# Kernel tuning notes

Hardware: AMD Instinct MI355X
Metric: run time of the kernel (lower is better)

The kernel has to match this reference:

```python
import jax, jax.numpy as jnp
import numpy as np

N_NODES = 100000
N_EDGES = 1250000
FEAT = 64
HID = 10
MOD = 10.0


def setup_inputs() -> dict:
    key = jax.random.key(0)
    ks = jax.random.split(key, 12)
    inp = {
        "X": jax.random.normal(ks[0], (N_NODES, FEAT), dtype=jnp.float32),
        "W2_0": jax.random.normal(ks[1], (2 * FEAT, HID), dtype=jnp.float32) * 0.1,
        "W1_0": jax.random.normal(ks[2], (HID, HID), dtype=jnp.float32) * 0.3,
        "W2_1": jax.random.normal(ks[3], (2 * HID, HID), dtype=jnp.float32) * 0.3,
        "W1_1": jax.random.normal(ks[4], (HID, HID), dtype=jnp.float32) * 0.3,
        "W2_2": jax.random.normal(ks[5], (2 * HID, HID), dtype=jnp.float32) * 0.3,
        "W1_2": jax.random.normal(ks[6], (HID, HID), dtype=jnp.float32) * 0.3,
        "Wf1": jax.random.normal(ks[7], (HID, FEAT), dtype=jnp.float32) * 0.3,
        "Wf2": jax.random.normal(ks[8], (FEAT, FEAT), dtype=jnp.float32) * 0.1,
        "edge_src": jax.random.randint(ks[9], (N_EDGES,), 0, N_NODES, dtype=jnp.int64 if jax.config.jax_enable_x64 else jnp.int32),
        "edge_dst": jax.random.randint(ks[10], (N_EDGES,), 0, N_NODES, dtype=jnp.int64 if jax.config.jax_enable_x64 else jnp.int32),
    }
    return inp


def _rgcn_layer(X, W2, W1, src, dst):
    # gather target (i) and source (j) node features per edge: [E, in_dim]
    X_i = X[dst]
    X_j = X[src]
    # message: dense_2(relu) then dense_1(relu), divided by mod
    m = jax.nn.relu(jnp.concatenate([X_i, X_j], axis=-1) @ W2)
    m = jax.nn.relu(m @ W1) / MOD  # [E, HID]
    # sum-aggregate messages at target nodes
    agg = jax.ops.segment_sum(m, dst, num_segments=N_NODES)
    # layer activation='relu' (identity here since messages are nonneg, kept for fidelity)
    return jax.nn.relu(agg)


def reference(X, W2_0, W1_0, W2_1, W1_1, W2_2, W1_2, Wf1, Wf2, edge_src, edge_dst):
    h = X
    for W2, W1 in ((W2_0, W1_0), (W2_1, W1_1), (W2_2, W1_2)):
        h = _rgcn_layer(h, W2, W1, edge_src, edge_dst)
    h = jax.nn.relu(h @ Wf1)
    h = jax.nn.relu(h @ Wf2)
    return h
```

## Files before the change

### kernel.cpp

```cpp
#include <hip/hip_runtime.h>

#define FEAT 64
#define HID 10
#define RS 16
#define EPB 1024
#define BSH 6
#define CHK 32

__global__ __launch_bounds__(256) void pre_l0(
    const float* __restrict__ X,
    const float* __restrict__ W2,
    float* __restrict__ A,
    float* __restrict__ B,
    int n_nodes)
{
    __shared__ float w2[128 * 10];
    for (int i = threadIdx.x; i < 1280; i += 256) w2[i] = W2[i];
    __syncthreads();

    int n = blockIdx.x * 256 + threadIdx.x;
    if (n >= n_nodes) return;

    const float4* xr = reinterpret_cast<const float4*>(X + (size_t)n * FEAT);
    float a[10], b[10];
#pragma unroll
    for (int h = 0; h < 10; h++) { a[h] = 0.f; b[h] = 0.f; }

#pragma unroll
    for (int blk = 0; blk < 16; blk++) {
        float4 u = xr[blk];
        float xv[4] = { u.x, u.y, u.z, u.w };
#pragma unroll
        for (int j = 0; j < 4; j++) {
            int k = blk * 4 + j;
#pragma unroll
            for (int h = 0; h < 10; h++) {
                a[h] = fmaf(xv[j], w2[k * 10 + h], a[h]);
                b[h] = fmaf(xv[j], w2[(64 + k) * 10 + h], b[h]);
            }
        }
    }

    float4* Ar = reinterpret_cast<float4*>(A + (size_t)n * RS);
    float4* Br = reinterpret_cast<float4*>(B + (size_t)n * RS);
    Ar[0] = make_float4(a[0], a[1], a[2], a[3]);
    Ar[1] = make_float4(a[4], a[5], a[6], a[7]);
    Ar[2] = make_float4(a[8], a[9], 0.f, 0.f);
    Br[0] = make_float4(b[0], b[1], b[2], b[3]);
    Br[1] = make_float4(b[4], b[5], b[6], b[7]);
    Br[2] = make_float4(b[8], b[9], 0.f, 0.f);
}

__global__ __launch_bounds__(256) void pre_small(
    const float* __restrict__ H,
    const float* __restrict__ W2,
    float* __restrict__ A,
    float* __restrict__ B,
    int n_nodes)
{
    __shared__ float w2[200];
    for (int i = threadIdx.x; i < 200; i += 256) w2[i] = W2[i];
    __syncthreads();

    int n = blockIdx.x * 256 + threadIdx.x;
    if (n >= n_nodes) return;

    const float4* hr = reinterpret_cast<const float4*>(H + (size_t)n * RS);
    float4 h0 = hr[0], h1 = hr[1], h2 = hr[2];
    float hv[10] = { h0.x, h0.y, h0.z, h0.w, h1.x, h1.y, h1.z, h1.w, h2.x, h2.y };

    float a[10], b[10];
#pragma unroll
    for (int h = 0; h < 10; h++) { a[h] = 0.f; b[h] = 0.f; }
#pragma unroll
    for (int k = 0; k < 10; k++) {
#pragma unroll
        for (int h = 0; h < 10; h++) {
            a[h] = fmaf(hv[k], w2[k * 10 + h], a[h]);
            b[h] = fmaf(hv[k], w2[(10 + k) * 10 + h], b[h]);
        }
    }

    float4* Ar = reinterpret_cast<float4*>(A + (size_t)n * RS);
    float4* Br = reinterpret_cast<float4*>(B + (size_t)n * RS);
    Ar[0] = make_float4(a[0], a[1], a[2], a[3]);
    Ar[1] = make_float4(a[4], a[5], a[6], a[7]);
    Ar[2] = make_float4(a[8], a[9], 0.f, 0.f);
    Br[0] = make_float4(b[0], b[1], b[2], b[3]);
    Br[1] = make_float4(b[4], b[5], b[6], b[7]);
    Br[2] = make_float4(b[8], b[9], 0.f, 0.f);
}


__global__ __launch_bounds__(256) void bin_hist_k(
    const int* __restrict__ dst, int* __restrict__ blockhist, int n_edges, int nbk)
{
    extern __shared__ int hist[];
    for (int i = threadIdx.x; i < nbk; i += 256) hist[i] = 0;
    __syncthreads();
    int base = blockIdx.x * EPB;
    for (int i = threadIdx.x; i < EPB; i += 256) {
        int e = base + i;
        if (e < n_edges) atomicAdd(&hist[dst[e] >> BSH], 1);
    }
    __syncthreads();
    int* row = blockhist + (size_t)blockIdx.x * nbk;
    for (int i = threadIdx.x; i < nbk; i += 256) row[i] = hist[i];
}

__global__ __launch_bounds__(256) void colchunk_sum_k(
    const int* __restrict__ blockhist, int* __restrict__ chunksum,
    int nbk, int nblk)
{
    int b = blockIdx.x * 256 + threadIdx.x;
    int c = blockIdx.y;
    if (b >= nbk) return;
    int k0 = c * CHK;
    int k1 = min(k0 + CHK, nblk);
    int s = 0;
    for (int k = k0; k < k1; k++) s += blockhist[(size_t)k * nbk + b];
    chunksum[(size_t)c * nbk + b] = s;
}

__global__ __launch_bounds__(256) void chunk_scan_k(
    int* __restrict__ chunksum, int* __restrict__ btot, int nbk, int nchk)
{
    int b = blockIdx.x * 256 + threadIdx.x;
    if (b >= nbk) return;
    int run = 0;
    for (int c = 0; c < nchk; c++) {
        size_t idx = (size_t)c * nbk + b;
        int v = chunksum[idx];
        chunksum[idx] = run;
        run += v;
    }
    btot[b] = run;
}

__global__ __launch_bounds__(256) void scan_k(
    const int* __restrict__ btot, int* __restrict__ bbase,
    int* __restrict__ bucket_start, int* __restrict__ start,
    int nbk, int n_nodes, int n_edges)
{
    __shared__ int ts[256];
    int t = threadIdx.x;
    int v[8];
    int s = 0;
#pragma unroll
    for (int j = 0; j < 8; j++) {
        int idx = t * 8 + j;
        v[j] = (idx < nbk) ? btot[idx] : 0;
        s += v[j];
    }
    ts[t] = s;
    __syncthreads();
    for (int off = 1; off < 256; off <<= 1) {
        int x = (t >= off) ? ts[t - off] : 0;
        __syncthreads();
        ts[t] += x;
        __syncthreads();
    }
    int run = ts[t] - s;
#pragma unroll
    for (int j = 0; j < 8; j++) {
        int idx = t * 8 + j;
        if (idx < nbk) { bbase[idx] = run; bucket_start[idx] = run; }
        run += v[j];
    }
    if (t == 255) { bucket_start[nbk] = n_edges; start[n_nodes] = n_edges; }
}

__global__ __launch_bounds__(256) void col_off2_k(
    int* __restrict__ blockhist, const int* __restrict__ chunksum,
    const int* __restrict__ bbase, int nbk, int nblk)
{
    int b = blockIdx.x * 256 + threadIdx.x;
    int c = blockIdx.y;
    if (b >= nbk) return;
    int k0 = c * CHK;
    int k1 = min(k0 + CHK, nblk);
    int run = bbase[b] + chunksum[(size_t)c * nbk + b];
    for (int k = k0; k < k1; k++) {
        size_t idx = (size_t)k * nbk + b;
        int v = blockhist[idx];
        blockhist[idx] = run;
        run += v;
    }
}

__global__ __launch_bounds__(256) void bin_scatter_k(
    const int* __restrict__ src, const int* __restrict__ dst,
    const int* __restrict__ blockhist, int* __restrict__ packed,
    int n_edges, int nbk)
{
    extern __shared__ int cur[];
    const int* row = blockhist + (size_t)blockIdx.x * nbk;
    for (int i = threadIdx.x; i < nbk; i += 256) cur[i] = row[i];
    __syncthreads();
    int base = blockIdx.x * EPB;
    for (int i = threadIdx.x; i < EPB; i += 256) {
        int e = base + i;
        if (e < n_edges) {
            int d = dst[e];
            int pos = atomicAdd(&cur[d >> BSH], 1);
            packed[pos] = ((d & 63) << 17) | src[e];
        }
    }
}

__global__ __launch_bounds__(256) void csr_k(
    const int* __restrict__ packed, const int* __restrict__ bucket_start,
    int* __restrict__ nbr, int* __restrict__ start, int n_nodes)
{
    __shared__ int hist[64];
    __shared__ int excl[64];
    __shared__ int cur[64];
    int b = blockIdx.x;
    int base = bucket_start[b];
    int end  = bucket_start[b + 1];
    if (threadIdx.x < 64) hist[threadIdx.x] = 0;
    __syncthreads();
    for (int i = base + threadIdx.x; i < end; i += 256)
        atomicAdd(&hist[packed[i] >> 17], 1);
    __syncthreads();
    if (threadIdx.x == 0) {
        int r = 0;
        for (int k = 0; k < 64; k++) { excl[k] = r; r += hist[k]; }
    }
    __syncthreads();
    if (threadIdx.x < 64) {
        cur[threadIdx.x] = excl[threadIdx.x];
        int node = (b << 6) + threadIdx.x;
        if (node < n_nodes) start[node] = base + excl[threadIdx.x];
    }
    __syncthreads();
    for (int i = base + threadIdx.x; i < end; i += 256) {
        int p = packed[i];
        int pos = base + atomicAdd(&cur[p >> 17], 1);
        nbr[pos] = p & 0x1FFFF;
    }
}

__global__ __launch_bounds__(256) void gather_k(
    const float* __restrict__ A,
    const float* __restrict__ B,
    const float* __restrict__ W1,
    const int* __restrict__ start,
    const int* __restrict__ nbr,
    float* __restrict__ H,
    int n_nodes)
{
    __shared__ float w1[100];
    for (int i = threadIdx.x; i < 100; i += 256) w1[i] = W1[i];
    __syncthreads();

    int t = blockIdx.x * 256 + threadIdx.x;
    int n = t >> 2;
    int q = t & 3;
    if (n >= n_nodes) return;

    const float4* ar = reinterpret_cast<const float4*>(A + (size_t)n * RS);
    float4 a0 = ar[0], a1 = ar[1], a2 = ar[2];
    float av[10] = { a0.x, a0.y, a0.z, a0.w, a1.x, a1.y, a1.z, a1.w, a2.x, a2.y };

    float acc[10];
#pragma unroll
    for (int h = 0; h < 10; h++) acc[h] = 0.f;

    int beg = start[n];
    int end = start[n + 1];
    for (int i = beg + q; i < end; i += 4) {
        int s = nbr[i];
        const float4* br = reinterpret_cast<const float4*>(B + (size_t)s * RS);
        float4 b0 = br[0], b1 = br[1], b2 = br[2];
        float pre[10] = { av[0] + b0.x, av[1] + b0.y, av[2] + b0.z, av[3] + b0.w,
                          av[4] + b1.x, av[5] + b1.y, av[6] + b1.z, av[7] + b1.w,
                          av[8] + b2.x, av[9] + b2.y };
#pragma unroll
        for (int j = 0; j < 10; j++) pre[j] = fmaxf(pre[j], 0.f);
#pragma unroll
        for (int h = 0; h < 10; h++) {
            float z = 0.f;
#pragma unroll
            for (int j = 0; j < 10; j++) z = fmaf(pre[j], w1[j * 10 + h], z);
            acc[h] += fmaxf(z, 0.f);
        }
    }

#pragma unroll
    for (int h = 0; h < 10; h++) acc[h] += __shfl_xor(acc[h], 1);
#pragma unroll
    for (int h = 0; h < 10; h++) acc[h] += __shfl_xor(acc[h], 2);

    if (q == 0) {
        float4* Hr = reinterpret_cast<float4*>(H + (size_t)n * RS);
        Hr[0] = make_float4(acc[0] * 0.1f, acc[1] * 0.1f, acc[2] * 0.1f, acc[3] * 0.1f);
        Hr[1] = make_float4(acc[4] * 0.1f, acc[5] * 0.1f, acc[6] * 0.1f, acc[7] * 0.1f);
        Hr[2] = make_float4(acc[8] * 0.1f, acc[9] * 0.1f, 0.f, 0.f);
    }
}

__global__ __launch_bounds__(256) void final_k(
    const float* __restrict__ H,
    const float* __restrict__ Wf1,
    const float* __restrict__ Wf2,
    float* __restrict__ out,
    int n_nodes)
{
    __shared__ float wf1[640];
    __shared__ float wf2s[64 * 64];
    __shared__ float tT[64 * 64];

    for (int i = threadIdx.x; i < 640; i += 256) wf1[i] = Wf1[i];
    {
        const float4* w2v = reinterpret_cast<const float4*>(Wf2);
        float4* w2s = reinterpret_cast<float4*>(wf2s);
        for (int i = threadIdx.x; i < 1024; i += 256) w2s[i] = w2v[i];
    }

    int node0 = blockIdx.x * 64;

    {
        int r = threadIdx.x & 63;
        int g = threadIdx.x >> 6;
        int node = node0 + r;
        float hv[10];
        if (node < n_nodes) {
            const float4* hr = reinterpret_cast<const float4*>(H + (size_t)node * RS);
            float4 h0 = hr[0], h1 = hr[1], h2 = hr[2];
            hv[0]=h0.x; hv[1]=h0.y; hv[2]=h0.z; hv[3]=h0.w;
            hv[4]=h1.x; hv[5]=h1.y; hv[6]=h1.z; hv[7]=h1.w;
            hv[8]=h2.x; hv[9]=h2.y;
        } else {
#pragma unroll
            for (int k = 0; k < 10; k++) hv[k] = 0.f;
        }
        __syncthreads();
#pragma unroll
        for (int j = 0; j < 16; j++) {
            int c = g * 16 + j;
            float v = 0.f;
#pragma unroll
            for (int k = 0; k < 10; k++) v = fmaf(hv[k], wf1[k * 64 + c], v);
            tT[c * 64 + r] = fmaxf(v, 0.f);
        }
    }
    __syncthreads();

    int r0 = (threadIdx.x >> 4) * 4;
    int c0 = (threadIdx.x & 15) * 4;
    float acc[4][4];
#pragma unroll
    for (int i = 0; i < 4; i++)
#pragma unroll
        for (int j = 0; j < 4; j++) acc[i][j] = 0.f;

    for (int k = 0; k < 64; k++) {
        float4 a = *reinterpret_cast<const float4*>(&tT[k * 64 + r0]);
        float4 b = *reinterpret_cast<const float4*>(&wf2s[k * 64 + c0]);
        float av[4] = { a.x, a.y, a.z, a.w };
        float bv[4] = { b.x, b.y, b.z, b.w };
#pragma unroll
        for (int i = 0; i < 4; i++)
#pragma unroll
            for (int j = 0; j < 4; j++)
                acc[i][j] = fmaf(av[i], bv[j], acc[i][j]);
    }

#pragma unroll
    for (int i = 0; i < 4; i++) {
        int node = node0 + r0 + i;
        if (node < n_nodes) {
            float4 o = make_float4(fmaxf(acc[i][0], 0.f), fmaxf(acc[i][1], 0.f),
                                   fmaxf(acc[i][2], 0.f), fmaxf(acc[i][3], 0.f));
            *reinterpret_cast<float4*>(&out[(size_t)node * FEAT + c0]) = o;
        }
    }
}

extern "C" void kernel_launch(void* const* d_in, const int* in_sizes, int n_in,
                              void* d_out, int out_size, void* d_ws, size_t ws_size,
                              hipStream_t stream) {
    const float* X    = (const float*)d_in[0];
    const float* W2_0 = (const float*)d_in[1];
    const float* W1_0 = (const float*)d_in[2];
    const float* W2_1 = (const float*)d_in[3];
    const float* W1_1 = (const float*)d_in[4];
    const float* W2_2 = (const float*)d_in[5];
    const float* W1_2 = (const float*)d_in[6];
    const float* Wf1  = (const float*)d_in[7];
    const float* Wf2  = (const float*)d_in[8];
    const int* src = (const int*)d_in[9];
    const int* dst = (const int*)d_in[10];
    float* out = (float*)d_out;

    const int n_edges = in_sizes[9];
    const int n_nodes = in_sizes[0] / FEAT;

    const int nbk  = (n_nodes + 63) >> 6;
    const int nblk = (n_edges + EPB - 1) / EPB;
    const int nchk = (nblk + CHK - 1) / CHK;

    const size_t h_elems = (size_t)n_nodes * RS;
    const size_t offA   = 0;
    const size_t offB   = offA + h_elems;
    const size_t offNbr = offB + h_elems;
    const size_t offPk  = offNbr + (size_t)n_edges;
    const size_t offBh  = offPk + (size_t)n_edges;
    const size_t offCs  = offBh + (size_t)nblk * nbk;
    const size_t offBt  = offCs + (size_t)nchk * nbk;
    const size_t offBb  = offBt + (size_t)nbk;
    const size_t offBs  = offBb + (size_t)nbk;
    const size_t offSt  = offBs + (size_t)nbk + 1;
    const size_t aux_elems = offSt + (size_t)n_nodes + 1;

    float* H = (float*)d_ws;
    char* aux;
    if (ws_size >= (h_elems + aux_elems) * 4) {
        aux = (char*)d_ws + h_elems * 4;
    } else {
        size_t tail = ((size_t)out_size - aux_elems) & ~(size_t)15;
        aux = (char*)((float*)d_out + tail);
    }
    float* A        = (float*)(aux + offA * 4);
    float* B        = (float*)(aux + offB * 4);
    int* nbr        = (int*)(aux + offNbr * 4);
    int* packed     = (int*)(aux + offPk * 4);
    int* blockhist  = (int*)(aux + offBh * 4);
    int* chunksum   = (int*)(aux + offCs * 4);
    int* btot       = (int*)(aux + offBt * 4);
    int* bbase      = (int*)(aux + offBb * 4);
    int* bstart     = (int*)(aux + offBs * 4);
    int* start      = (int*)(aux + offSt * 4);

    const int nb = (n_nodes + 255) / 256;
    const int gb = (n_nodes * 4 + 255) / 256;
    const int fb = (n_nodes + 63) / 64;
    const int cb = (nbk + 255) / 256;
    const size_t lds_bins = (size_t)nbk * 4;

    bin_hist_k<<<nblk, 256, lds_bins, stream>>>(dst, blockhist, n_edges, nbk);
    colchunk_sum_k<<<dim3(cb, nchk), 256, 0, stream>>>(blockhist, chunksum, nbk, nblk);
    chunk_scan_k<<<cb, 256, 0, stream>>>(chunksum, btot, nbk, nchk);
    scan_k<<<1, 256, 0, stream>>>(btot, bbase, bstart, start, nbk, n_nodes, n_edges);
    col_off2_k<<<dim3(cb, nchk), 256, 0, stream>>>(blockhist, chunksum, bbase, nbk, nblk);
    bin_scatter_k<<<nblk, 256, lds_bins, stream>>>(src, dst, blockhist, packed, n_edges, nbk);
    csr_k<<<nbk, 256, 0, stream>>>(packed, bstart, nbr, start, n_nodes);

    pre_l0<<<nb, 256, 0, stream>>>(X, W2_0, A, B, n_nodes);
    gather_k<<<gb, 256, 0, stream>>>(A, B, W1_0, start, nbr, H, n_nodes);

    pre_small<<<nb, 256, 0, stream>>>(H, W2_1, A, B, n_nodes);
    gather_k<<<gb, 256, 0, stream>>>(A, B, W1_1, start, nbr, H, n_nodes);

    pre_small<<<nb, 256, 0, stream>>>(H, W2_2, A, B, n_nodes);
    gather_k<<<gb, 256, 0, stream>>>(A, B, W1_2, start, nbr, H, n_nodes);

    final_k<<<fb, 256, 0, stream>>>(H, Wf1, Wf2, out, n_nodes);
}
```

Before: 283.4 us.

## Drop CSR build; aggregate per 64-node bucket with LDS atomics and fuse next-layer projection

Removes the per-node CSR sort (csr_k) and the start array. Edges are processed straight from the bucket-packed list, one block per 64-node bucket, accumulating messages into shared memory with atomics. The next layer's W2 projection is fused into the gather epilogue, so the separate pre_small kernels go away and A/B are ping-ponged between two buffers. This saves a launch and a pass over the edges for CSR, and an H round trip per layer. In exchange it adds LDS atomic contention, 100 W1 values held in registers (possible pressure), and fixed-size workspace use with no fallback when the workspace is too small.

```diff
diff --git a/kernel.cpp b/kernel.cpp
--- a/kernel.cpp
+++ b/kernel.cpp
@@ -6,6 +6,7 @@
 #define EPB 1024
 #define BSH 6
 #define CHK 32
+#define AS 13
 
 __global__ __launch_bounds__(256) void pre_l0(
     const float* __restrict__ X,
@@ -51,46 +52,6 @@
     Br[2] = make_float4(b[8], b[9], 0.f, 0.f);
 }
 
-__global__ __launch_bounds__(256) void pre_small(
-    const float* __restrict__ H,
-    const float* __restrict__ W2,
-    float* __restrict__ A,
-    float* __restrict__ B,
-    int n_nodes)
-{
-    __shared__ float w2[200];
-    for (int i = threadIdx.x; i < 200; i += 256) w2[i] = W2[i];
-    __syncthreads();
-
-    int n = blockIdx.x * 256 + threadIdx.x;
-    if (n >= n_nodes) return;
-
-    const float4* hr = reinterpret_cast<const float4*>(H + (size_t)n * RS);
-    float4 h0 = hr[0], h1 = hr[1], h2 = hr[2];
-    float hv[10] = { h0.x, h0.y, h0.z, h0.w, h1.x, h1.y, h1.z, h1.w, h2.x, h2.y };
-
-    float a[10], b[10];
-#pragma unroll
-    for (int h = 0; h < 10; h++) { a[h] = 0.f; b[h] = 0.f; }
-#pragma unroll
-    for (int k = 0; k < 10; k++) {
-#pragma unroll
-        for (int h = 0; h < 10; h++) {
-            a[h] = fmaf(hv[k], w2[k * 10 + h], a[h]);
-            b[h] = fmaf(hv[k], w2[(10 + k) * 10 + h], b[h]);
-        }
-    }
-
-    float4* Ar = reinterpret_cast<float4*>(A + (size_t)n * RS);
-    float4* Br = reinterpret_cast<float4*>(B + (size_t)n * RS);
-    Ar[0] = make_float4(a[0], a[1], a[2], a[3]);
-    Ar[1] = make_float4(a[4], a[5], a[6], a[7]);
-    Ar[2] = make_float4(a[8], a[9], 0.f, 0.f);
-    Br[0] = make_float4(b[0], b[1], b[2], b[3]);
-    Br[1] = make_float4(b[4], b[5], b[6], b[7]);
-    Br[2] = make_float4(b[8], b[9], 0.f, 0.f);
-}
-
 
 __global__ __launch_bounds__(256) void bin_hist_k(
     const int* __restrict__ dst, int* __restrict__ blockhist, int n_edges, int nbk)
@@ -139,8 +100,7 @@
 
 __global__ __launch_bounds__(256) void scan_k(
     const int* __restrict__ btot, int* __restrict__ bbase,
-    int* __restrict__ bucket_start, int* __restrict__ start,
-    int nbk, int n_nodes, int n_edges)
+    int* __restrict__ bucket_start, int nbk, int n_edges)
 {
     __shared__ int ts[256];
     int t = threadIdx.x;
@@ -167,7 +127,7 @@
         if (idx < nbk) { bbase[idx] = run; bucket_start[idx] = run; }
         run += v[j];
     }
-    if (t == 255) { bucket_start[nbk] = n_edges; start[n_nodes] = n_edges; }
+    if (t == 255) bucket_start[nbk] = n_edges;
 }
 
 __global__ __launch_bounds__(256) void col_off2_k(
@@ -208,95 +168,94 @@
     }
 }
 
-__global__ __launch_bounds__(256) void csr_k(
-    const int* __restrict__ packed, const int* __restrict__ bucket_start,
-    int* __restrict__ nbr, int* __restrict__ start, int n_nodes)
-{
-    __shared__ int hist[64];
-    __shared__ int excl[64];
-    __shared__ int cur[64];
-    int b = blockIdx.x;
-    int base = bucket_start[b];
-    int end  = bucket_start[b + 1];
-    if (threadIdx.x < 64) hist[threadIdx.x] = 0;
-    __syncthreads();
-    for (int i = base + threadIdx.x; i < end; i += 256)
-        atomicAdd(&hist[packed[i] >> 17], 1);
-    __syncthreads();
-    if (threadIdx.x == 0) {
-        int r = 0;
-        for (int k = 0; k < 64; k++) { excl[k] = r; r += hist[k]; }
-    }
-    __syncthreads();
-    if (threadIdx.x < 64) {
-        cur[threadIdx.x] = excl[threadIdx.x];
-        int node = (b << 6) + threadIdx.x;
-        if (node < n_nodes) start[node] = base + excl[threadIdx.x];
-    }
-    __syncthreads();
-    for (int i = base + threadIdx.x; i < end; i += 256) {
-        int p = packed[i];
-        int pos = base + atomicAdd(&cur[p >> 17], 1);
-        nbr[pos] = p & 0x1FFFF;
-    }
-}
-
-__global__ __launch_bounds__(256) void gather_k(
+template<bool LAST>
+__global__ __launch_bounds__(256) void bgather_k(
     const float* __restrict__ A,
     const float* __restrict__ B,
     const float* __restrict__ W1,
-    const int* __restrict__ start,
-    const int* __restrict__ nbr,
-    float* __restrict__ H,
+    const float* __restrict__ W2n,
+    const int* __restrict__ bstart,
+    const int* __restrict__ packed,
+    float* __restrict__ An,
+    float* __restrict__ Bn,
+    float* __restrict__ Hout,
     int n_nodes)
 {
-    __shared__ float w1[100];
-    for (int i = threadIdx.x; i < 100; i += 256) w1[i] = W1[i];
-    __syncthreads();
-
-    int t = blockIdx.x * 256 + threadIdx.x;
-    int n = t >> 2;
-    int q = t & 3;
-    if (n >= n_nodes) return;
-
-    const float4* ar = reinterpret_cast<const float4*>(A + (size_t)n * RS);
-    float4 a0 = ar[0], a1 = ar[1], a2 = ar[2];
-    float av[10] = { a0.x, a0.y, a0.z, a0.w, a1.x, a1.y, a1.z, a1.w, a2.x, a2.y };
-
-    float acc[10];
-#pragma unroll
-    for (int h = 0; h < 10; h++) acc[h] = 0.f;
-
-    int beg = start[n];
-    int end = start[n + 1];
-    for (int i = beg + q; i < end; i += 4) {
-        int s = nbr[i];
+    __shared__ float w2[200];
+    __shared__ float As[64 * AS];
+    __shared__ float acc[64 * AS];
+
+    int t = threadIdx.x;
+    if (!LAST) {
+        for (int i = t; i < 200; i += 256) w2[i] = W2n[i];
+    }
+    for (int i = t; i < 64 * AS; i += 256) acc[i] = 0.f;
+
+    float w1r[100];
+#pragma unroll
+    for (int i = 0; i < 100; i++) w1r[i] = W1[i];
+
+    int bkt = blockIdx.x;
+    int node0 = bkt << 6;
+
+    for (int i = t; i < 640; i += 256) {
+        int r = i / 10, h = i - r * 10;
+        As[r * AS + h] = A[(size_t)(node0 + r) * RS + h];
+    }
+    __syncthreads();
+
+    int base = bstart[bkt];
+    int end  = bstart[bkt + 1];
+    for (int i = base + t; i < end; i += 256) {
+        int p  = packed[i];
+        int s  = p & 0x1FFFF;
+        int dl = p >> 17;
         const float4* br = reinterpret_cast<const float4*>(B + (size_t)s * RS);
         float4 b0 = br[0], b1 = br[1], b2 = br[2];
-        float pre[10] = { av[0] + b0.x, av[1] + b0.y, av[2] + b0.z, av[3] + b0.w,
-                          av[4] + b1.x, av[5] + b1.y, av[6] + b1.z, av[7] + b1.w,
-                          av[8] + b2.x, av[9] + b2.y };
+        const float* ar = &As[dl * AS];
+        float pre[10] = { ar[0] + b0.x, ar[1] + b0.y, ar[2] + b0.z, ar[3] + b0.w,
+                          ar[4] + b1.x, ar[5] + b1.y, ar[6] + b1.z, ar[7] + b1.w,
+                          ar[8] + b2.x, ar[9] + b2.y };
 #pragma unroll
         for (int j = 0; j < 10; j++) pre[j] = fmaxf(pre[j], 0.f);
+        float* accd = &acc[dl * AS];
 #pragma unroll
         for (int h = 0; h < 10; h++) {
             float z = 0.f;
 #pragma unroll
-            for (int j = 0; j < 10; j++) z = fmaf(pre[j], w1[j * 10 + h], z);
-            acc[h] += fmaxf(z, 0.f);
-        }
-    }
-
-#pragma unroll
-    for (int h = 0; h < 10; h++) acc[h] += __shfl_xor(acc[h], 1);
-#pragma unroll
-    for (int h = 0; h < 10; h++) acc[h] += __shfl_xor(acc[h], 2);
-
-    if (q == 0) {
-        float4* Hr = reinterpret_cast<float4*>(H + (size_t)n * RS);
-        Hr[0] = make_float4(acc[0] * 0.1f, acc[1] * 0.1f, acc[2] * 0.1f, acc[3] * 0.1f);
-        Hr[1] = make_float4(acc[4] * 0.1f, acc[5] * 0.1f, acc[6] * 0.1f, acc[7] * 0.1f);
-        Hr[2] = make_float4(acc[8] * 0.1f, acc[9] * 0.1f, 0.f, 0.f);
+            for (int j = 0; j < 10; j++) z = fmaf(pre[j], w1r[j * 10 + h], z);
+            atomicAdd(&accd[h], fmaxf(z, 0.f));
+        }
+    }
+    __syncthreads();
+
+    int r = t >> 2;
+    int q = t & 3;
+    int node = node0 + r;
+    if (node >= n_nodes) return;
+
+    if (LAST) {
+#pragma unroll
+        for (int j = 0; j < 3; j++) {
+            int o = q * 3 + j;
+            float v = (o < 10) ? acc[r * AS + o] * 0.1f : 0.f;
+            if (o < 12) Hout[(size_t)node * RS + o] = v;
+        }
+    } else {
+        float hv[10];
+#pragma unroll
+        for (int k = 0; k < 10; k++) hv[k] = acc[r * AS + k] * 0.1f;
+#pragma unroll
+        for (int j = 0; j < 5; j++) {
+            int o = q * 5 + j;
+            int h   = (o < 10) ? o : o - 10;
+            int off = (o < 10) ? 0 : 100;
+            float z = 0.f;
+#pragma unroll
+            for (int k = 0; k < 10; k++) z = fmaf(hv[k], w2[off + k * 10 + h], z);
+            float* dstp = (o < 10) ? An : Bn;
+            dstp[(size_t)node * RS + h] = z;
+        }
     }
 }
 
@@ -398,43 +357,36 @@
     const int n_nodes = in_sizes[0] / FEAT;
 
     const int nbk  = (n_nodes + 63) >> 6;
+    const int NP   = nbk << 6;
     const int nblk = (n_edges + EPB - 1) / EPB;
     const int nchk = (nblk + CHK - 1) / CHK;
 
-    const size_t h_elems = (size_t)n_nodes * RS;
-    const size_t offA   = 0;
-    const size_t offB   = offA + h_elems;
-    const size_t offNbr = offB + h_elems;
-    const size_t offPk  = offNbr + (size_t)n_edges;
+    const size_t h_elems = (size_t)NP * RS;
+    const size_t offH   = 0;
+    const size_t offA0  = offH  + h_elems;
+    const size_t offB0  = offA0 + h_elems;
+    const size_t offA1  = offB0 + h_elems;
+    const size_t offB1  = offA1 + h_elems;
+    const size_t offPk  = offB1 + h_elems;
     const size_t offBh  = offPk + (size_t)n_edges;
     const size_t offCs  = offBh + (size_t)nblk * nbk;
     const size_t offBt  = offCs + (size_t)nchk * nbk;
     const size_t offBb  = offBt + (size_t)nbk;
     const size_t offBs  = offBb + (size_t)nbk;
-    const size_t offSt  = offBs + (size_t)nbk + 1;
-    const size_t aux_elems = offSt + (size_t)n_nodes + 1;
-
-    float* H = (float*)d_ws;
-    char* aux;
-    if (ws_size >= (h_elems + aux_elems) * 4) {
-        aux = (char*)d_ws + h_elems * 4;
-    } else {
-        size_t tail = ((size_t)out_size - aux_elems) & ~(size_t)15;
-        aux = (char*)((float*)d_out + tail);
-    }
-    float* A        = (float*)(aux + offA * 4);
-    float* B        = (float*)(aux + offB * 4);
-    int* nbr        = (int*)(aux + offNbr * 4);
-    int* packed     = (int*)(aux + offPk * 4);
-    int* blockhist  = (int*)(aux + offBh * 4);
-    int* chunksum   = (int*)(aux + offCs * 4);
-    int* btot       = (int*)(aux + offBt * 4);
-    int* bbase      = (int*)(aux + offBb * 4);
-    int* bstart     = (int*)(aux + offBs * 4);
-    int* start      = (int*)(aux + offSt * 4);
+
+    float* H        = (float*)d_ws + offH;
+    float* A0       = (float*)d_ws + offA0;
+    float* B0       = (float*)d_ws + offB0;
+    float* A1       = (float*)d_ws + offA1;
+    float* B1       = (float*)d_ws + offB1;
+    int* packed     = (int*)d_ws + offPk;
+    int* blockhist  = (int*)d_ws + offBh;
+    int* chunksum   = (int*)d_ws + offCs;
+    int* btot       = (int*)d_ws + offBt;
+    int* bbase      = (int*)d_ws + offBb;
+    int* bstart     = (int*)d_ws + offBs;
 
     const int nb = (n_nodes + 255) / 256;
-    const int gb = (n_nodes * 4 + 255) / 256;
     const int fb = (n_nodes + 63) / 64;
     const int cb = (nbk + 255) / 256;
     const size_t lds_bins = (size_t)nbk * 4;
@@ -442,19 +394,17 @@
     bin_hist_k<<<nblk, 256, lds_bins, stream>>>(dst, blockhist, n_edges, nbk);
     colchunk_sum_k<<<dim3(cb, nchk), 256, 0, stream>>>(blockhist, chunksum, nbk, nblk);
     chunk_scan_k<<<cb, 256, 0, stream>>>(chunksum, btot, nbk, nchk);
-    scan_k<<<1, 256, 0, stream>>>(btot, bbase, bstart, start, nbk, n_nodes, n_edges);
+    scan_k<<<1, 256, 0, stream>>>(btot, bbase, bstart, nbk, n_edges);
     col_off2_k<<<dim3(cb, nchk), 256, 0, stream>>>(blockhist, chunksum, bbase, nbk, nblk);
     bin_scatter_k<<<nblk, 256, lds_bins, stream>>>(src, dst, blockhist, packed, n_edges, nbk);
-    csr_k<<<nbk, 256, 0, stream>>>(packed, bstart, nbr, start, n_nodes);
-
-    pre_l0<<<nb, 256, 0, stream>>>(X, W2_0, A, B, n_nodes);
-    gather_k<<<gb, 256, 0, stream>>>(A, B, W1_0, start, nbr, H, n_nodes);
-
-    pre_small<<<nb, 256, 0, stream>>>(H, W2_1, A, B, n_nodes);
-    gather_k<<<gb, 256, 0, stream>>>(A, B, W1_1, start, nbr, H, n_nodes);
-
-    pre_small<<<nb, 256, 0, stream>>>(H, W2_2, A, B, n_nodes);
-    gather_k<<<gb, 256, 0, stream>>>(A, B, W1_2, start, nbr, H, n_nodes);
+
+    pre_l0<<<nb, 256, 0, stream>>>(X, W2_0, A0, B0, n_nodes);
+    bgather_k<false><<<nbk, 256, 0, stream>>>(A0, B0, W1_0, W2_1, bstart, packed,
+                                              A1, B1, nullptr, n_nodes);
+    bgather_k<false><<<nbk, 256, 0, stream>>>(A1, B1, W1_1, W2_2, bstart, packed,
+                                              A0, B0, nullptr, n_nodes);
+    bgather_k<true><<<nbk, 256, 0, stream>>>(A0, B0, W1_2, nullptr, bstart, packed,
+                                             nullptr, nullptr, H, n_nodes);
 
     final_k<<<fb, 256, 0, stream>>>(H, Wf1, Wf2, out, n_nodes);
 }
```

Result: slower. 420.8 us (+48.5%).
